# Optimization experiments

Hardware: AMD Instinct MI355X
Metric: run time of the kernel (lower is better)

Reference implementation:

```python
import jax, jax.numpy as jnp
import numpy as np
from jax import lax

B, C, H, W = 8, 384, 32, 32
HEADS, G, STRIDE, KSIZE = 12, 6, 2, 3
HC = C // HEADS          # head channels = 32
CG = C // G              # group channels = 64
NGH = HEADS // G         # heads per group = 2
DEPTHS = 2
D2 = C * 4               # MLP hidden
HK, WK = H // STRIDE, W // STRIDE
NS = HK * WK             # deformable samples = 256
SCALE = HC ** -0.5


def dwconv(x, w, b, stride=1, pad=1):
    # depthwise conv, x:(N,Cx,H,W), w:(Cx,kh,kw)
    c = x.shape[1]
    y = lax.conv_general_dilated(x, w[:, None], (stride, stride),
                                 [(pad, pad), (pad, pad)], feature_group_count=c,
                                 dimension_numbers=('NCHW', 'OIHW', 'NCHW'))
    return y + b[None, :, None, None]


def conv1x1(x, w, b=None):
    y = jnp.einsum('oc,bchw->bohw', w, x)
    return y if b is None else y + b[None, :, None, None]


def layernorm_c(x, w, b, eps=1e-5):
    # LayerNormProxy: LN over channel dim of NCHW
    xt = x.transpose(0, 2, 3, 1)
    mu = xt.mean(-1, keepdims=True)
    var = xt.var(-1, keepdims=True)
    xt = (xt - mu) * lax.rsqrt(var + eps) * w + b
    return xt.transpose(0, 3, 1, 2)


def grid_sample(img, grid):
    # F.grid_sample, bilinear, align_corners=True. img:(N,Ci,Hi,Wi), grid:(N,Hg,Wg,2) as (x,y) in [-1,1]
    N, Ci, Hi, Wi = img.shape
    gx = (grid[..., 0] + 1.0) * 0.5 * (Wi - 1)
    gy = (grid[..., 1] + 1.0) * 0.5 * (Hi - 1)
    x0 = jnp.floor(gx)
    y0 = jnp.floor(gy)
    wx = (gx - x0)[:, None]   # (N,1,Hg,Wg)
    wy = (gy - y0)[:, None]
    x0i = jnp.clip(x0.astype(jnp.int32), 0, Wi - 1)
    y0i = jnp.clip(y0.astype(jnp.int32), 0, Hi - 1)
    x1i = jnp.clip(x0i + 1, 0, Wi - 1)
    y1i = jnp.clip(y0i + 1, 0, Hi - 1)
    gather = jax.vmap(lambda im, yi, xi: im[:, yi, xi])  # -> (N,Ci,Hg,Wg)
    v00 = gather(img, y0i, x0i)
    v01 = gather(img, y0i, x1i)
    v10 = gather(img, y1i, x0i)
    v11 = gather(img, y1i, x1i)
    return (v00 * (1 - wx) * (1 - wy) + v01 * wx * (1 - wy)
            + v10 * (1 - wx) * wy + v11 * wx * wy)


def _norm_grid(hs, ws, centered):
    if centered:  # _get_ref_points
        ys = jnp.linspace(0.5, hs - 0.5, hs)
        xs = jnp.linspace(0.5, ws - 0.5, ws)
    else:         # _get_q_grid
        ys = jnp.arange(hs, dtype=jnp.float32)
        xs = jnp.arange(ws, dtype=jnp.float32)
    ys = ys / (hs - 1.0) * 2.0 - 1.0
    xs = xs / (ws - 1.0) * 2.0 - 1.0
    return jnp.stack(jnp.meshgrid(ys, xs, indexing='ij'), -1)  # (hs,ws,2) (y,x)


def dattn(x, wq, bq, wk, bk, wv, bv, wo, bo, odw, odb, olw, olb, opw, rpe):
    q = conv1x1(x, wq, bq)                              # (B,C,H,W)
    q_off = q.reshape(B * G, CG, H, W)
    off = dwconv(q_off, odw, odb, stride=STRIDE, pad=KSIZE // 2)  # (BG,CG,HK,WK)
    off = jax.nn.gelu(layernorm_c(off, olw, olb), approximate=False)
    off = conv1x1(off, opw).transpose(0, 2, 3, 1)       # (BG,HK,WK,2) as (dy,dx)
    ref = _norm_grid(HK, WK, True)[None]
    pos = jnp.clip(off + ref, -1.0, 1.0)                # (BG,HK,WK,2) (y,x)
    xs = grid_sample(x.reshape(B * G, CG, H, W), pos[..., ::-1])  # (BG,CG,HK,WK)
    xs = xs.reshape(B, C, 1, NS)
    qf = q.reshape(B * HEADS, HC, H * W)
    k = conv1x1(xs, wk, bk).reshape(B * HEADS, HC, NS)
    v = conv1x1(xs, wv, bv).reshape(B * HEADS, HC, NS)
    attn = jnp.einsum('bcm,bcn->bmn', qf, k) * SCALE    # (B*HEADS, HW, NS)
    rpe_g = jnp.broadcast_to(rpe[None], (B,) + rpe.shape).reshape(B * G, NGH, 2 * H - 1, 2 * W - 1)
    qg = _norm_grid(H, W, False).reshape(1, H * W, 2)
    disp = (qg[:, :, None, :] - pos.reshape(B * G, 1, NS, 2)) * 0.5  # (BG,HW,NS,2)
    bias = grid_sample(rpe_g, disp[..., ::-1]).reshape(B * HEADS, H * W, NS)
    attn = jax.nn.softmax(attn + bias, axis=2)
    out = jnp.einsum('bmn,bcn->bcm', attn, v).reshape(B, C, H, W)
    return conv1x1(out, wo, bo)


def _forward(x, lpu_w, lpu_b, wq, bq, wk, bk, wv, bv, wo, bo,
             off_dw_w, off_dw_b, off_ln_w, off_ln_b, off_pw_w, rpe,
             mlp_w1, mlp_b1, mlp_dw_w, mlp_dw_b, mlp_w2, mlp_b2):
    # proj is Identity (dim_in == dim_embed); layer_norms/layer_scales/drop_path are Identity; dropouts are 0
    for d in range(DEPTHS):
        x = x + dwconv(x, lpu_w[d], lpu_b[d])  # local perception unit
        x = x + dattn(x, wq[d], bq[d], wk[d], bk[d], wv[d], bv[d], wo[d], bo[d],
                      off_dw_w[d], off_dw_b[d], off_ln_w[d], off_ln_b[d], off_pw_w[d], rpe[d])
        h = conv1x1(x, mlp_w1[d], mlp_b1[d])
        h = h + dwconv(h, mlp_dw_w[d], mlp_dw_b[d])
        h = jax.nn.gelu(h, approximate=False)
        x = x + conv1x1(h, mlp_w2[d], mlp_b2[d])
    return x


def setup_inputs():
    key = jax.random.key(0)
    ks = iter(jax.random.split(key, 16))
    def p(shape, std=0.02):
        return jax.random.normal(next(ks), shape, jnp.float32) * std
    D = DEPTHS
    return {
        "x": jax.random.normal(next(ks), (B, C, H, W), jnp.float32),
        "lpu_w": p((D, C, 3, 3)), "lpu_b": jnp.zeros((D, C), jnp.float32),
        "wq": p((D, C, C)), "bq": jnp.zeros((D, C), jnp.float32),
        "wk": p((D, C, C)), "bk": jnp.zeros((D, C), jnp.float32),
        "wv": p((D, C, C)), "bv": jnp.zeros((D, C), jnp.float32),
        "wo": p((D, C, C)), "bo": jnp.zeros((D, C), jnp.float32),
        "off_dw_w": p((D, CG, 3, 3)), "off_dw_b": jnp.zeros((D, CG), jnp.float32),
        "off_ln_w": jnp.ones((D, CG), jnp.float32), "off_ln_b": jnp.zeros((D, CG), jnp.float32),
        "off_pw_w": p((D, 2, CG)),
        "rpe": p((D, HEADS, 2 * H - 1, 2 * W - 1), 0.01),
        "mlp_w1": p((D, D2, C)), "mlp_b1": jnp.zeros((D, D2), jnp.float32),
        "mlp_dw_w": p((D, D2, 3, 3)), "mlp_dw_b": jnp.zeros((D, D2), jnp.float32),
        "mlp_w2": p((D, C, D2)), "mlp_b2": jnp.zeros((D, C), jnp.float32),
    }


def reference(x, lpu_w, lpu_b, wq, bq, wk, bk, wv, bv, wo, bo,
              off_dw_w, off_dw_b, off_ln_w, off_ln_b, off_pw_w, rpe,
              mlp_w1, mlp_b1, mlp_dw_w, mlp_dw_b, mlp_w2, mlp_b2):
    return _forward(x, lpu_w, lpu_b, wq, bq, wk, bk, wv, bv, wo, bo,
                    off_dw_w, off_dw_b, off_ln_w, off_ln_b, off_pw_w, rpe,
                    mlp_w1, mlp_b1, mlp_dw_w, mlp_dw_b, mlp_w2, mlp_b2)
```

## Files before the change

### kernel.cpp

```cpp
#include <hip/hip_runtime.h>
#include <hip/hip_bf16.h>
#include <math.h>

namespace {

constexpr int B_ = 8, C_ = 384, H_ = 32, W_ = 32, HW_ = 1024;
constexpr int HEADS_ = 12, G_ = 6, HC_ = 32, CG_ = 64, NS_ = 256, D2_ = 1536;
constexpr float SCALE_ = 0.17677669529663687f;

using short8 = __attribute__((ext_vector_type(8))) short;
using f32x4 = __attribute__((ext_vector_type(4))) float;
using u32x4 = __attribute__((ext_vector_type(4))) unsigned;
typedef unsigned short ushort_t;

__device__ __forceinline__ float gelu_exact(float x) {
  return 0.5f * x * (1.f + erff(x * 0.70710678118654752f));
}
__device__ __forceinline__ ushort_t f2bf(float f) {
  unsigned u = __float_as_uint(f);
  u = (u + 0x7FFFu + ((u >> 16) & 1u)) >> 16;
  return (ushort_t)u;
}
__device__ __forceinline__ float bf2f(ushort_t s) {
  return __uint_as_float(((unsigned)s) << 16);
}
__device__ __forceinline__ float bflo(unsigned u) { return __uint_as_float(u << 16); }
__device__ __forceinline__ float bfhi(unsigned u) { return __uint_as_float(u & 0xFFFF0000u); }
__device__ __forceinline__ unsigned pack2(float a, float b) {
  return (unsigned)f2bf(a) | ((unsigned)f2bf(b) << 16);
}

typedef __attribute__((address_space(1))) const unsigned int gq_u32;
typedef __attribute__((address_space(3))) unsigned int lq_u32;
__device__ __forceinline__ void gload16(const ushort_t* g, ushort_t* l) {
  __builtin_amdgcn_global_load_lds((gq_u32*)g, (lq_u32*)l, 16, 0, 0);
}

__global__ __launch_bounds__(256) void wcvt_rpe(
    const float* __restrict__ s0, const float* __restrict__ s1,
    const float* __restrict__ s2, const float* __restrict__ s3,
    const float* __restrict__ s4, const float* __restrict__ s5,
    ushort_t* __restrict__ dst, const float* __restrict__ rpe,
    uint2* __restrict__ rpq) {
  int blk = blockIdx.x;
  if (blk < 13824) {
    long idx = (long)blk * 256 + threadIdx.x;
    long off = idx;
    const float* s;
    if (off < 294912) s = s0;
    else if ((off -= 294912) < 294912) s = s1;
    else if ((off -= 294912) < 294912) s = s2;
    else if ((off -= 294912) < 294912) s = s3;
    else if ((off -= 294912) < 1179648) s = s4;
    else { off -= 1179648; s = s5; }
    dst[idx] = f2bf(s[off]);
  } else {
    int hb = blk - 13824;
    const float* rph = rpe + (size_t)hb * 3969;
    uint2* dq = rpq + (size_t)hb * 4096;
    for (int i = threadIdx.x; i < 4096; i += 256) {
      int y = i >> 6, x = i & 63;
      float v00 = 0.f, v01 = 0.f, v10 = 0.f, v11 = 0.f;
      if (y < 63) {
        if (x < 63) v00 = rph[y * 63 + x];
        if (x < 62) v01 = rph[y * 63 + x + 1];
      }
      if (y < 62) {
        if (x < 63) v10 = rph[(y + 1) * 63 + x];
        if (x < 62) v11 = rph[(y + 1) * 63 + x + 1];
      }
      dq[i] = make_uint2(pack2(v00, v01), pack2(v10, v11));
    }
  }
}

__global__ __launch_bounds__(256) void dwconv_lpu(
    const float* __restrict__ x, const float* __restrict__ w,
    const float* __restrict__ bias, float* __restrict__ y,
    ushort_t* __restrict__ yt) {
  __shared__ __align__(16) float tile[32][33];
  int hp = blockIdx.x, c0 = blockIdx.y * 32, b = blockIdx.z;
  int t = threadIdx.x;
  int cl = t >> 3, g4 = t & 7;
  int c = c0 + cl;
  const float* img = x + ((size_t)b * C_ + c) * HW_;
  const float* wc = w + c * 9;
  float o0 = bias[c], o1 = o0, o2 = o0, o3 = o0;
#pragma unroll
  for (int ky = 0; ky < 3; ++ky) {
    int ih = hp + ky - 1;
    if ((unsigned)ih >= 32u) continue;
    const float* row = img + ih * 32 + g4 * 4;
    float4 m = *(const float4*)row;
    float v0 = (g4 > 0) ? row[-1] : 0.f;
    float v5 = (g4 < 7) ? row[4] : 0.f;
    float k0 = wc[ky * 3], k1 = wc[ky * 3 + 1], k2 = wc[ky * 3 + 2];
    o0 = fmaf(k0, v0, fmaf(k1, m.x, fmaf(k2, m.y, o0)));
    o1 = fmaf(k0, m.x, fmaf(k1, m.y, fmaf(k2, m.z, o1)));
    o2 = fmaf(k0, m.y, fmaf(k1, m.z, fmaf(k2, m.w, o2)));
    o3 = fmaf(k0, m.z, fmaf(k1, m.w, fmaf(k2, v5, o3)));
  }
  float4 ctr = *(const float4*)(img + hp * 32 + g4 * 4);
  o0 += ctr.x; o1 += ctr.y; o2 += ctr.z; o3 += ctr.w;
  *(float4*)(y + ((size_t)b * C_ + c) * HW_ + hp * 32 + g4 * 4) =
      make_float4(o0, o1, o2, o3);
  tile[cl][g4 * 4 + 0] = o0;
  tile[cl][g4 * 4 + 1] = o1;
  tile[cl][g4 * 4 + 2] = o2;
  tile[cl][g4 * 4 + 3] = o3;
  __syncthreads();
  int wl = t >> 3, cg = t & 7;
  unsigned p0 = pack2(tile[cg * 4 + 0][wl], tile[cg * 4 + 1][wl]);
  unsigned p1 = pack2(tile[cg * 4 + 2][wl], tile[cg * 4 + 3][wl]);
  unsigned* dst = (unsigned*)(yt + ((size_t)b * HW_ + hp * 32 + wl) * C_ + c0 + cg * 4);
  dst[0] = p0;
  dst[1] = p1;
}

__global__ __launch_bounds__(256) void dwgelu_t(
    const ushort_t* __restrict__ hin, const float* __restrict__ w,
    const float* __restrict__ bias, ushort_t* __restrict__ ht) {
  __shared__ __align__(16) float tile[2][32][33];
  int hp0 = blockIdx.x * 2, c0 = blockIdx.y * 32, b = blockIdx.z;
  int t = threadIdx.x;
  int cl = t >> 3, rw = (t >> 2) & 1, g8 = t & 3;
  int hp = hp0 + rw;
  int c = c0 + cl;
  const ushort_t* img = hin + ((size_t)b * D2_ + c) * HW_;
  const float* wc = w + c * 9;
  float o[8];
  float bi = bias[c];
#pragma unroll
  for (int j = 0; j < 8; ++j) o[j] = bi;
#pragma unroll
  for (int ky = 0; ky < 3; ++ky) {
    int ih = hp + ky - 1;
    if ((unsigned)ih >= 32u) continue;
    const ushort_t* row = img + ih * 32 + g8 * 8;
    uint4 u = *(const uint4*)row;
    float vv[10];
    vv[0] = (g8 > 0) ? bf2f(row[-1]) : 0.f;
    vv[1] = bflo(u.x); vv[2] = bfhi(u.x); vv[3] = bflo(u.y); vv[4] = bfhi(u.y);
    vv[5] = bflo(u.z); vv[6] = bfhi(u.z); vv[7] = bflo(u.w); vv[8] = bfhi(u.w);
    vv[9] = (g8 < 3) ? bf2f(row[8]) : 0.f;
    float k0 = wc[ky * 3], k1 = wc[ky * 3 + 1], k2 = wc[ky * 3 + 2];
#pragma unroll
    for (int j = 0; j < 8; ++j)
      o[j] = fmaf(k0, vv[j], fmaf(k1, vv[j + 1], fmaf(k2, vv[j + 2], o[j])));
  }
  {
    uint4 u = *(const uint4*)(img + hp * 32 + g8 * 8);
    float cv[8] = {bflo(u.x), bfhi(u.x), bflo(u.y), bfhi(u.y),
                   bflo(u.z), bfhi(u.z), bflo(u.w), bfhi(u.w)};
#pragma unroll
    for (int j = 0; j < 8; ++j) {
      o[j] += cv[j];
      tile[rw][cl][g8 * 8 + j] = gelu_exact(o[j]);
    }
  }
  __syncthreads();
  int wl = t >> 3, cg = t & 7;
#pragma unroll
  for (int rr = 0; rr < 2; ++rr) {
    unsigned p0 = pack2(tile[rr][cg * 4 + 0][wl], tile[rr][cg * 4 + 1][wl]);
    unsigned p1 = pack2(tile[rr][cg * 4 + 2][wl], tile[rr][cg * 4 + 3][wl]);
    unsigned* dst = (unsigned*)(ht + ((size_t)b * HW_ + (hp0 + rr) * 32 + wl) * D2_ + c0 + cg * 4);
    dst[0] = p0;
    dst[1] = p1;
  }
}

__global__ __launch_bounds__(256) void gemm_kv(
    const ushort_t* __restrict__ Wk, const ushort_t* __restrict__ Wv,
    const ushort_t* __restrict__ Xt, const float* __restrict__ bk,
    const float* __restrict__ bv, ushort_t* __restrict__ ktb,
    ushort_t* __restrict__ vbn) {
  constexpr int K = C_, N = NS_, O = C_;
  struct __align__(16) SMem {
    union {
      struct { char a[8192]; char b[8192]; } st;
      float shuf[64 * 68];
    };
  };
  __shared__ SMem sm;
  int t = threadIdx.x;
  int lane = t & 63, wave = t >> 6;
  int wm = (wave >> 1) * 32, wn = (wave & 1) * 32;
  int bz = blockIdx.z;
  bool isK = blockIdx.y < 6;
  int o0 = (isK ? blockIdx.y : blockIdx.y - 6) * 64;
  int n0 = blockIdx.x * 64;
  const ushort_t* Wb = isK ? Wk : Wv;
  const float* bias = isK ? bk : bv;
  const ushort_t* Ag = Wb + (size_t)o0 * K;
  const ushort_t* Bg = Xt + ((size_t)bz * N + n0) * K;
  int sr = t >> 3, sc = t & 7;
  int swz = ((sc ^ (sr & 7)) << 4);
  f32x4 acc[2][2];
#pragma unroll
  for (int fi = 0; fi < 2; ++fi)
#pragma unroll
    for (int fj = 0; fj < 2; ++fj) acc[fi][fj] = f32x4{0.f, 0.f, 0.f, 0.f};
  int lrow = lane & 15, lk = lane >> 4;
  short8 a0 = *(const short8*)(Ag + (size_t)sr * K + sc * 8);
  short8 a1 = *(const short8*)(Ag + (size_t)(sr + 32) * K + sc * 8);
  short8 b0 = *(const short8*)(Bg + (size_t)sr * K + sc * 8);
  short8 b1 = *(const short8*)(Bg + (size_t)(sr + 32) * K + sc * 8);
  constexpr int NSTEP = K / 64;
#pragma unroll
  for (int s = 0; s < NSTEP; ++s) {
    if (s) __syncthreads();
    *(short8*)(sm.st.a + sr * 128 + swz) = a0;
    *(short8*)(sm.st.a + (sr + 32) * 128 + swz) = a1;
    *(short8*)(sm.st.b + sr * 128 + swz) = b0;
    *(short8*)(sm.st.b + (sr + 32) * 128 + swz) = b1;
    __syncthreads();
    if (s + 1 < NSTEP) {
      int k0 = (s + 1) * 64;
      a0 = *(const short8*)(Ag + (size_t)sr * K + k0 + sc * 8);
      a1 = *(const short8*)(Ag + (size_t)(sr + 32) * K + k0 + sc * 8);
      b0 = *(const short8*)(Bg + (size_t)sr * K + k0 + sc * 8);
      b1 = *(const short8*)(Bg + (size_t)(sr + 32) * K + k0 + sc * 8);
    }
#pragma unroll
    for (int kk = 0; kk < 2; ++kk) {
      short8 af[2], bfr[2];
#pragma unroll
      for (int fi = 0; fi < 2; ++fi) {
        int row = wm + fi * 16 + lrow;
        af[fi] = *(const short8*)(sm.st.a + row * 128 + (((kk * 4 + lk) ^ (row & 7)) << 4));
      }
#pragma unroll
      for (int fj = 0; fj < 2; ++fj) {
        int row = wn + fj * 16 + lrow;
        bfr[fj] = *(const short8*)(sm.st.b + row * 128 + (((kk * 4 + lk) ^ (row & 7)) << 4));
      }
#pragma unroll
      for (int fi = 0; fi < 2; ++fi)
#pragma unroll
        for (int fj = 0; fj < 2; ++fj)
          acc[fi][fj] = __builtin_amdgcn_mfma_f32_16x16x32_bf16(af[fi], bfr[fj], acc[fi][fj], 0, 0, 0);
    }
  }
  __syncthreads();
#pragma unroll
  for (int fi = 0; fi < 2; ++fi) {
#pragma unroll
    for (int r = 0; r < 4; ++r) {
      int ol = wm + fi * 16 + lk * 4 + r;
      float bi = bias[o0 + ol];
#pragma unroll
      for (int fj = 0; fj < 2; ++fj) {
        int nl = wn + fj * 16 + lrow;
        sm.shuf[ol * 68 + nl] = acc[fi][fj][r] + bi;
      }
    }
  }
  __syncthreads();
  if (isK) {
    int nl = t >> 2, og = (t & 3) * 16;
    unsigned pk[8];
#pragma unroll
    for (int i = 0; i < 8; ++i)
      pk[i] = pack2(sm.shuf[(og + 2 * i) * 68 + nl], sm.shuf[(og + 2 * i + 1) * 68 + nl]);
    unsigned* dst = (unsigned*)(ktb + ((size_t)bz * N + (n0 + nl)) * O + o0 + og);
    *(uint4*)(dst) = make_uint4(pk[0], pk[1], pk[2], pk[3]);
    *(uint4*)(dst + 4) = make_uint4(pk[4], pk[5], pk[6], pk[7]);
  } else {
    int ol = t >> 2, ng = (t & 3) * 16;
    unsigned pk[8];
#pragma unroll
    for (int i = 0; i < 8; ++i)
      pk[i] = pack2(sm.shuf[ol * 68 + ng + 2 * i], sm.shuf[ol * 68 + ng + 2 * i + 1]);
    unsigned* dst = (unsigned*)(vbn + ((size_t)bz * O + (o0 + ol)) * N + n0 + ng);
    *(uint4*)(dst) = make_uint4(pk[0], pk[1], pk[2], pk[3]);
    *(uint4*)(dst + 4) = make_uint4(pk[4], pk[5], pk[6], pk[7]);
  }
}

template <int BN, bool F32, bool B16N, bool B16T, bool RES>
__global__ __launch_bounds__(256) void gemm128(
    const ushort_t* __restrict__ Wb, const ushort_t* __restrict__ Xt,
    const float* __restrict__ bias, const float* __restrict__ resid,
    float* __restrict__ Y, ushort_t* __restrict__ Yb, int O, int K, int N) {
  constexpr int MFW = (BN == 128) ? 4 : 2;
  __shared__ __align__(16) ushort_t sA[2][128 * 64];
  __shared__ __align__(16) ushort_t sB[2][BN * 64];
  int t = threadIdx.x;
  int l = t & 63, w = t >> 6;
  int o0 = blockIdx.y * 128, n0 = blockIdx.x * BN, bz = blockIdx.z;
  const ushort_t* Ag = Wb + (size_t)o0 * K;
  const ushort_t* Bg = Xt + ((size_t)bz * N + n0) * K;
  int lr8 = l >> 3;
  int scol = (((l & 7) ^ (lr8 & 7)) * 8);
  int lrow = l & 15, lg = l >> 4;
  int wm = (BN == 128) ? (w >> 1) * 64 : w * 32;
  int wn = (BN == 128) ? (w & 1) * 64 : 0;
  f32x4 acc[MFW][4];
#pragma unroll
  for (int fi = 0; fi < MFW; ++fi)
#pragma unroll
    for (int fj = 0; fj < 4; ++fj) acc[fi][fj] = f32x4{0.f, 0.f, 0.f, 0.f};
  auto stage = [&](int buf, int k0) {
#pragma unroll
    for (int i = 0; i < 4; ++i)
      gload16(Ag + (size_t)(w * 32 + i * 8 + lr8) * K + k0 + scol,
              sA[buf] + (w * 32 + i * 8) * 64);
    if constexpr (BN == 128) {
#pragma unroll
      for (int i = 0; i < 4; ++i)
        gload16(Bg + (size_t)(w * 32 + i * 8 + lr8) * K + k0 + scol,
                sB[buf] + (w * 32 + i * 8) * 64);
    } else {
#pragma unroll
      for (int i = 0; i < 2; ++i)
        gload16(Bg + (size_t)(w * 16 + i * 8 + lr8) * K + k0 + scol,
                sB[buf] + (w * 16 + i * 8) * 64);
    }
  };
  stage(0, 0);
  __syncthreads();
  int nstep = K >> 6;
  for (int s = 0; s < nstep; ++s) {
    int cur = s & 1;
    if (s + 1 < nstep) stage(cur ^ 1, (s + 1) * 64);
#pragma unroll
    for (int kk = 0; kk < 2; ++kk) {
      short8 af[MFW], bfr[4];
#pragma unroll
      for (int fi = 0; fi < MFW; ++fi) {
        int row = wm + fi * 16 + lrow;
        af[fi] = *(const short8*)(sA[cur] + row * 64 + (((kk * 4 + lg) ^ (row & 7)) << 3));
      }
#pragma unroll
      for (int fj = 0; fj < 4; ++fj) {
        int row = wn + fj * 16 + lrow;
        bfr[fj] = *(const short8*)(sB[cur] + row * 64 + (((kk * 4 + lg) ^ (row & 7)) << 3));
      }
#pragma unroll
      for (int fi = 0; fi < MFW; ++fi)
#pragma unroll
        for (int fj = 0; fj < 4; ++fj)
          acc[fi][fj] = __builtin_amdgcn_mfma_f32_16x16x32_bf16(af[fi], bfr[fj], acc[fi][fj], 0, 0, 0);
    }
    __syncthreads();
  }
#pragma unroll
  for (int fi = 0; fi < MFW; ++fi) {
    int ob = wm + fi * 16 + lg * 4;
    float bi[4];
#pragma unroll
    for (int r = 0; r < 4; ++r) bi[r] = bias[o0 + ob + r];
#pragma unroll
    for (int fj = 0; fj < 4; ++fj) {
      int n = n0 + wn + fj * 16 + lrow;
      float v[4];
#pragma unroll
      for (int r = 0; r < 4; ++r) {
        v[r] = acc[fi][fj][r] + bi[r];
        if (RES) v[r] += resid[((size_t)bz * O + ob + r + o0) * N + n];
        if (F32) Y[((size_t)bz * O + ob + r + o0) * N + n] = v[r];
        if (B16N) Yb[((size_t)bz * O + ob + r + o0) * N + n] = f2bf(v[r]);
      }
      if (B16T) {
        uint2 u;
        u.x = pack2(v[0], v[1]);
        u.y = pack2(v[2], v[3]);
        *(uint2*)&Yb[((size_t)bz * N + n) * O + o0 + ob] = u;
      }
    }
  }
}

__global__ __launch_bounds__(256) void offset_kernel(
    const ushort_t* __restrict__ qt, const float* __restrict__ odw,
    const float* __restrict__ odb, const float* __restrict__ olw,
    const float* __restrict__ olb, const float* __restrict__ opw,
    float* __restrict__ pos) {
  int blk = blockIdx.x;
  int bg = blk >> 2, pb = blk & 3;
  int b = bg / G_, g = bg % G_;
  int t = threadIdx.x;
  int p = pb * 64 + (t >> 2);
  int q = t & 3;
  int c0 = q * 16;
  int hk = p >> 4, wk = p & 15;
  const ushort_t* qb = qt + (size_t)b * HW_ * C_ + g * CG_ + c0;
  float sv[16];
#pragma unroll
  for (int j = 0; j < 16; ++j) sv[j] = odb[c0 + j];
#pragma unroll
  for (int ky = 0; ky < 3; ++ky) {
    int ih = 2 * hk + ky - 1;
    if ((unsigned)ih >= 32u) continue;
#pragma unroll
    for (int kx = 0; kx < 3; ++kx) {
      int iw = 2 * wk + kx - 1;
      if ((unsigned)iw >= 32u) continue;
      const ushort_t* qp = qb + (size_t)(ih * 32 + iw) * C_;
      uint4 u0 = *(const uint4*)qp;
      uint4 u1 = *(const uint4*)(qp + 8);
      float vv[16] = {bflo(u0.x), bfhi(u0.x), bflo(u0.y), bfhi(u0.y),
                      bflo(u0.z), bfhi(u0.z), bflo(u0.w), bfhi(u0.w),
                      bflo(u1.x), bfhi(u1.x), bflo(u1.y), bfhi(u1.y),
                      bflo(u1.z), bfhi(u1.z), bflo(u1.w), bfhi(u1.w)};
      int tap = ky * 3 + kx;
#pragma unroll
      for (int j = 0; j < 16; ++j)
        sv[j] = fmaf(odw[(c0 + j) * 9 + tap], vv[j], sv[j]);
    }
  }
  float s1 = 0.f;
#pragma unroll
  for (int j = 0; j < 16; ++j) s1 += sv[j];
  s1 += __shfl_xor(s1, 1);
  s1 += __shfl_xor(s1, 2);
  float mu = s1 * (1.f / CG_);
  float vs = 0.f;
#pragma unroll
  for (int j = 0; j < 16; ++j) {
    float d = sv[j] - mu;
    vs = fmaf(d, d, vs);
  }
  vs += __shfl_xor(vs, 1);
  vs += __shfl_xor(vs, 2);
  float rs = rsqrtf(vs * (1.f / CG_) + 1e-5f);
  float dy = 0.f, dx = 0.f;
#pragma unroll
  for (int j = 0; j < 16; ++j) {
    int c = c0 + j;
    float tv = (sv[j] - mu) * rs * olw[c] + olb[c];
    float ge = gelu_exact(tv);
    dy = fmaf(opw[c], ge, dy);
    dx = fmaf(opw[CG_ + c], ge, dx);
  }
  dy += __shfl_xor(dy, 1);
  dy += __shfl_xor(dy, 2);
  dx += __shfl_xor(dx, 1);
  dx += __shfl_xor(dx, 2);
  if (q == 0) {
    float ry = (hk + 0.5f) * (2.f / 15.f) - 1.f;
    float rx = (wk + 0.5f) * (2.f / 15.f) - 1.f;
    pos[(size_t)bg * 512 + p * 2 + 0] = fminf(fmaxf(dy + ry, -1.f), 1.f);
    pos[(size_t)bg * 512 + p * 2 + 1] = fminf(fmaxf(dx + rx, -1.f), 1.f);
  }
}

__global__ __launch_bounds__(256) void sample_xst(
    const float* __restrict__ y1, const float* __restrict__ pos,
    ushort_t* __restrict__ xst) {
  int bg = blockIdx.y;
  int b = bg / G_, g = bg % G_;
  int t = threadIdx.x;
  int cg = t & 63, nl = t >> 6;
  int n = blockIdx.x * 4 + nl;
  float py = pos[(size_t)bg * 512 + 2 * n];
  float px = pos[(size_t)bg * 512 + 2 * n + 1];
  float gx = (px + 1.f) * 15.5f, gy = (py + 1.f) * 15.5f;
  float fx = floorf(gx), fy = floorf(gy);
  float wx = gx - fx, wy = gy - fy;
  int x0 = min(max((int)fx, 0), 31), y0 = min(max((int)fy, 0), 31);
  int x1 = min(x0 + 1, 31), y1i = min(y0 + 1, 31);
  const float* img = y1 + ((size_t)b * C_ + g * CG_ + cg) * HW_;
  float v00 = img[y0 * 32 + x0], v01 = img[y0 * 32 + x1];
  float v10 = img[y1i * 32 + x0], v11 = img[y1i * 32 + x1];
  float v = v00 * (1.f - wx) * (1.f - wy) + v01 * wx * (1.f - wy) +
            v10 * (1.f - wx) * wy + v11 * wx * wy;
  xst[((size_t)b * NS_ + n) * C_ + g * CG_ + cg] = f2bf(v);
}

__global__ __launch_bounds__(256) void attn_kernel(
    const ushort_t* __restrict__ qt, const ushort_t* __restrict__ kt,
    const ushort_t* __restrict__ vbn, const float* __restrict__ pos,
    const uint2* __restrict__ rpq, ushort_t* __restrict__ aot) {
  __shared__ __align__(16) uint2 sRPQ[4096];
  __shared__ __align__(16) ushort_t sP[4][32 * 40];
  __shared__ unsigned sIB[256];
  __shared__ float sW2[512];
  int bid = blockIdx.x;
  int swzb = (bid & 7) * 96 + (bid >> 3);
  int qb = swzb & 7;
  int grp = swzb >> 3;
  int h = grp % HEADS_;
  int b = grp / HEADS_;
  int t = threadIdx.x;
  int l = t & 63, wv = t >> 6;
  int lrow = l & 15, lg = l >> 4;
  int bg = b * G_ + (h >> 1);
  {
    const ushort_t* src = (const ushort_t*)(rpq + (size_t)h * 4096);
    ushort_t* dstb = (ushort_t*)sRPQ;
#pragma unroll
    for (int i = 0; i < 8; ++i)
      gload16(src + i * 2048 + t * 8, dstb + i * 2048 + wv * 512);
  }
  {
    float py = pos[(size_t)bg * 512 + 2 * t];
    float px = pos[(size_t)bg * 512 + 2 * t + 1];
    float cy = 15.5f - 15.5f * py;
    float cx = 15.5f - 15.5f * px;
    float fy = floorf(cy), fx = floorf(cx);
    sIB[t] = (unsigned)((int)fy * 64 + (int)fx);
    sW2[2 * t] = cy - fy;
    sW2[2 * t + 1] = cx - fx;
  }
  __syncthreads();

  int m0 = qb * 128 + wv * 32;
  short8 qf[2];
  int aq[2];
#pragma unroll
  for (int f = 0; f < 2; ++f) {
    int m = m0 + f * 16 + lrow;
    qf[f] = *(const short8*)(qt + ((size_t)b * HW_ + m) * C_ + h * HC_ + lg * 8);
    aq[f] = (m >> 5) * 64 + (m & 31);
  }
  const ushort_t* kbase = kt + (size_t)b * NS_ * C_ + h * HC_;
  const ushort_t* vbase = vbn + ((size_t)b * C_ + h * HC_) * NS_;
  f32x4 oc[2][2];
#pragma unroll
  for (int f = 0; f < 2; ++f)
#pragma unroll
    for (int ct = 0; ct < 2; ++ct) oc[f][ct] = f32x4{0.f, 0.f, 0.f, 0.f};
  float mrun[2] = {-1e30f, -1e30f}, lrun[2] = {0.f, 0.f};
  ushort_t* sPw = sP[wv];

  for (int c = 0; c < 8; ++c) {
    f32x4 s[2][2];
    __builtin_amdgcn_s_setprio(1);
#pragma unroll
    for (int T = 0; T < 2; ++T) {
      short8 kf = *(const short8*)(kbase + (size_t)((c * 2 + T) * 16 + lrow) * C_ + lg * 8);
#pragma unroll
      for (int f = 0; f < 2; ++f)
        s[f][T] = __builtin_amdgcn_mfma_f32_16x16x32_bf16(kf, qf[f], f32x4{0.f, 0.f, 0.f, 0.f}, 0, 0, 0);
    }
    __builtin_amdgcn_s_setprio(0);
    u32x4 ibT[2];
    f32x4 wA[2], wB[2];
#pragma unroll
    for (int T = 0; T < 2; ++T) {
      int kbase2 = c * 32 + T * 16 + lg * 4;
      ibT[T] = *(const u32x4*)&sIB[kbase2];
      wA[T] = *(const f32x4*)&sW2[2 * kbase2];
      wB[T] = *(const f32x4*)&sW2[2 * kbase2 + 4];
    }
#pragma unroll
    for (int f = 0; f < 2; ++f)
#pragma unroll
      for (int T = 0; T < 2; ++T)
#pragma unroll
        for (int r = 0; r < 4; ++r) {
          int a = aq[f] + (int)ibT[T][r];
          float wy = (r < 2) ? wA[T][(r & 1) * 2] : wB[T][(r & 1) * 2];
          float wx = (r < 2) ? wA[T][(r & 1) * 2 + 1] : wB[T][(r & 1) * 2 + 1];
          uint2 qd = sRPQ[a];
          float b00 = bflo(qd.x), b01 = bfhi(qd.x);
          float b10 = bflo(qd.y), b11 = bfhi(qd.y);
          float r0 = b00 + wx * (b01 - b00);
          float r1 = b10 + wx * (b11 - b10);
          s[f][T][r] = s[f][T][r] * SCALE_ + r0 + wy * (r1 - r0);
        }
#pragma unroll
    for (int f = 0; f < 2; ++f) {
      float mx = s[f][0][0];
#pragma unroll
      for (int T = 0; T < 2; ++T)
#pragma unroll
        for (int r = 0; r < 4; ++r) mx = fmaxf(mx, s[f][T][r]);
      mx = fmaxf(mx, __shfl_xor(mx, 16));
      mx = fmaxf(mx, __shfl_xor(mx, 32));
      if (!__all(mx <= mrun[f] + 8.f)) {
        float newm = fmaxf(mrun[f], mx);
        float fac = __expf(mrun[f] - newm);
        mrun[f] = newm;
        lrun[f] *= fac;
#pragma unroll
        for (int ct = 0; ct < 2; ++ct)
#pragma unroll
          for (int r = 0; r < 4; ++r) oc[f][ct][r] *= fac;
      }
      float ps = 0.f;
#pragma unroll
      for (int T = 0; T < 2; ++T)
#pragma unroll
        for (int r = 0; r < 4; ++r) {
          float p = __expf(s[f][T][r] - mrun[f]);
          s[f][T][r] = p;
          ps += p;
        }
      ps += __shfl_xor(ps, 16);
      ps += __shfl_xor(ps, 32);
      lrun[f] += ps;
#pragma unroll
      for (int T = 0; T < 2; ++T) {
        uint2 u;
        u.x = pack2(s[f][T][0], s[f][T][1]);
        u.y = pack2(s[f][T][2], s[f][T][3]);
        *(uint2*)&sPw[(f * 16 + lrow) * 40 + T * 16 + lg * 4] = u;
      }
    }
    short8 pa[2];
#pragma unroll
    for (int f = 0; f < 2; ++f)
      pa[f] = *(const short8*)&sPw[(f * 16 + lrow) * 40 + lg * 8];
    __builtin_amdgcn_s_setprio(1);
#pragma unroll
    for (int ct = 0; ct < 2; ++ct) {
      short8 vf = *(const short8*)(vbase + (size_t)(ct * 16 + lrow) * NS_ + c * 32 + lg * 8);
#pragma unroll
      for (int f = 0; f < 2; ++f)
        oc[f][ct] = __builtin_amdgcn_mfma_f32_16x16x32_bf16(pa[f], vf, oc[f][ct], 0, 0, 0);
    }
    __builtin_amdgcn_s_setprio(0);
  }
#pragma unroll
  for (int f = 0; f < 2; ++f) {
    float inv = 1.f / lrun[f];
    float invq[4];
#pragma unroll
    for (int r = 0; r < 4; ++r) invq[r] = __shfl(inv, lg * 4 + r);
#pragma unroll
    for (int ct = 0; ct < 2; ++ct)
#pragma unroll
      for (int r = 0; r < 4; ++r) {
        int m = m0 + f * 16 + lg * 4 + r;
        aot[((size_t)b * HW_ + m) * C_ + h * HC_ + ct * 16 + lrow] =
            f2bf(oc[f][ct][r] * invq[r]);
      }
  }
}

}

extern "C" void kernel_launch(void* const* d_in, const int* in_sizes, int n_in,
                              void* d_out, int out_size, void* d_ws,
                              size_t ws_size, hipStream_t stream) {
  const float* x_in = (const float*)d_in[0];
  const float* lpu_w = (const float*)d_in[1];
  const float* lpu_b = (const float*)d_in[2];
  const float* wq = (const float*)d_in[3];
  const float* bq = (const float*)d_in[4];
  const float* wk = (const float*)d_in[5];
  const float* bk = (const float*)d_in[6];
  const float* wv = (const float*)d_in[7];
  const float* bv = (const float*)d_in[8];
  const float* wo = (const float*)d_in[9];
  const float* bo = (const float*)d_in[10];
  const float* odw = (const float*)d_in[11];
  const float* odb = (const float*)d_in[12];
  const float* olw = (const float*)d_in[13];
  const float* olb = (const float*)d_in[14];
  const float* opw = (const float*)d_in[15];
  const float* rpe = (const float*)d_in[16];
  const float* w1 = (const float*)d_in[17];
  const float* b1 = (const float*)d_in[18];
  const float* mdw = (const float*)d_in[19];
  const float* mdb = (const float*)d_in[20];
  const float* w2 = (const float*)d_in[21];
  const float* b2 = (const float*)d_in[22];
  float* out = (float*)d_out;

  constexpr size_t XSZ = (size_t)B_ * C_ * HW_;
  constexpr size_t SSZ = (size_t)B_ * C_ * NS_;
  constexpr size_t HSZ = (size_t)B_ * D2_ * HW_;

  char* base = (char*)d_ws;
  auto alloc = [&](size_t bytes) {
    char* p = base;
    base += (bytes + 255) & ~(size_t)255;
    return p;
  };
  float* bufX = (float*)alloc(XSZ * 4);
  float* y1 = (float*)alloc(XSZ * 4);
  float* x2 = (float*)alloc(XSZ * 4);
  float* pos = (float*)alloc(48 * 512 * 4);
  ushort_t* qt = (ushort_t*)alloc(XSZ * 2);
  ushort_t* tb1 = (ushort_t*)alloc(XSZ * 2);
  ushort_t* aot = (ushort_t*)alloc(XSZ * 2);
  ushort_t* xst = (ushort_t*)alloc(SSZ * 2);
  ushort_t* ktb = (ushort_t*)alloc(SSZ * 2);
  ushort_t* vbn = (ushort_t*)alloc(SSZ * 2);
  ushort_t* h1b = (ushort_t*)alloc(HSZ * 2);
  ushort_t* h3t = (ushort_t*)alloc(HSZ * 2);
  ushort_t* wb = (ushort_t*)alloc((size_t)3538944 * 2);
  uint2* rpq = (uint2*)alloc((size_t)2 * HEADS_ * 4096 * 8);

  ushort_t* wqb = wb;
  ushort_t* wkb = wb + 294912;
  ushort_t* wvb = wb + 589824;
  ushort_t* wob = wb + 884736;
  ushort_t* w1b = wb + 1179648;
  ushort_t* w2b = wb + 2359296;

  wcvt_rpe<<<13824 + 24, 256, 0, stream>>>(wq, wk, wv, wo, w1, w2, wb, rpe, rpq);

  for (int d = 0; d < 2; ++d) {
    const float* xin = (d == 0) ? x_in : bufX;
    float* xnext = (d == 1) ? out : bufX;
    const ushort_t* wqd = wqb + (size_t)d * 147456;
    const ushort_t* wkd = wkb + (size_t)d * 147456;
    const ushort_t* wvd = wvb + (size_t)d * 147456;
    const ushort_t* wod = wob + (size_t)d * 147456;
    const ushort_t* w1d = w1b + (size_t)d * 589824;
    const ushort_t* w2d = w2b + (size_t)d * 589824;

    dwconv_lpu<<<dim3(32, 12, 8), 256, 0, stream>>>(xin, lpu_w + d * C_ * 9,
                                                    lpu_b + d * C_, y1, tb1);
    gemm128<64, false, false, true, false><<<dim3(16, 3, 8), 256, 0, stream>>>(
        wqd, tb1, bq + d * C_, nullptr, nullptr, qt, C_, C_, HW_);
    offset_kernel<<<192, 256, 0, stream>>>(qt, odw + d * CG_ * 9, odb + d * CG_,
                                           olw + d * CG_, olb + d * CG_,
                                           opw + d * 2 * CG_, pos);
    sample_xst<<<dim3(64, 48), 256, 0, stream>>>(y1, pos, xst);
    gemm_kv<<<dim3(4, 12, 8), 256, 0, stream>>>(wkd, wvd, xst, bk + d * C_,
                                                bv + d * C_, ktb, vbn);
    attn_kernel<<<768, 256, 0, stream>>>(qt, ktb, vbn, pos,
                                         rpq + (size_t)d * HEADS_ * 4096, aot);
    gemm128<64, true, false, true, true><<<dim3(16, 3, 8), 256, 0, stream>>>(
        wod, aot, bo + d * C_, y1, x2, tb1, C_, C_, HW_);
    gemm128<128, false, true, false, false><<<dim3(8, 12, 8), 256, 0, stream>>>(
        w1d, tb1, b1 + d * D2_, nullptr, nullptr, h1b, D2_, C_, HW_);
    dwgelu_t<<<dim3(16, 48, 8), 256, 0, stream>>>(h1b, mdw + d * D2_ * 9,
                                                  mdb + d * D2_, h3t);
    gemm128<64, true, false, false, true><<<dim3(16, 3, 8), 256, 0, stream>>>(
        w2d, h3t, b2 + d * C_, x2, xnext, nullptr, C_, D2_, HW_);
  }
}
```

Baseline: 432.6 us.

## Store intermediate residual activations in bf16 and halve RPE table size

Switches the fp32 residual/intermediate activations (y1, x2, block output between depths) to bf16, so the dwconv, sample, output-projection and MLP GEMM epilogues read and write half the bytes. The relative-position table is also stored as single packed pairs, with the second row read from a +64 offset instead of a quad-packed entry, which halves the LDS footprint and the load in the attention kernel. The cost is lower precision on the residual stream and an extra LDS read per bias lookup.

```diff
diff --git a/kernel.cpp b/kernel.cpp
--- a/kernel.cpp
+++ b/kernel.cpp
@@ -41,7 +41,7 @@
     const float* __restrict__ s2, const float* __restrict__ s3,
     const float* __restrict__ s4, const float* __restrict__ s5,
     ushort_t* __restrict__ dst, const float* __restrict__ rpe,
-    uint2* __restrict__ rpq) {
+    unsigned* __restrict__ rp2) {
   int blk = blockIdx.x;
   if (blk < 13824) {
     long idx = (long)blk * 256 + threadIdx.x;
@@ -57,53 +57,64 @@
   } else {
     int hb = blk - 13824;
     const float* rph = rpe + (size_t)hb * 3969;
-    uint2* dq = rpq + (size_t)hb * 4096;
+    unsigned* dq = rp2 + (size_t)hb * 4096;
     for (int i = threadIdx.x; i < 4096; i += 256) {
       int y = i >> 6, x = i & 63;
-      float v00 = 0.f, v01 = 0.f, v10 = 0.f, v11 = 0.f;
+      float v0 = 0.f, v1 = 0.f;
       if (y < 63) {
-        if (x < 63) v00 = rph[y * 63 + x];
-        if (x < 62) v01 = rph[y * 63 + x + 1];
-      }
-      if (y < 62) {
-        if (x < 63) v10 = rph[(y + 1) * 63 + x];
-        if (x < 62) v11 = rph[(y + 1) * 63 + x + 1];
-      }
-      dq[i] = make_uint2(pack2(v00, v01), pack2(v10, v11));
-    }
-  }
-}
-
+        if (x < 63) v0 = rph[y * 63 + x];
+        if (x < 62) v1 = rph[y * 63 + x + 1];
+      }
+      dq[i] = pack2(v0, v1);
+    }
+  }
+}
+
+template <bool INF32>
 __global__ __launch_bounds__(256) void dwconv_lpu(
-    const float* __restrict__ x, const float* __restrict__ w,
-    const float* __restrict__ bias, float* __restrict__ y,
+    const void* __restrict__ xin, const float* __restrict__ w,
+    const float* __restrict__ bias, ushort_t* __restrict__ yb,
     ushort_t* __restrict__ yt) {
   __shared__ __align__(16) float tile[32][33];
   int hp = blockIdx.x, c0 = blockIdx.y * 32, b = blockIdx.z;
   int t = threadIdx.x;
   int cl = t >> 3, g4 = t & 7;
   int c = c0 + cl;
-  const float* img = x + ((size_t)b * C_ + c) * HW_;
   const float* wc = w + c * 9;
   float o0 = bias[c], o1 = o0, o2 = o0, o3 = o0;
+  float m0, m1, m2, m3;
 #pragma unroll
   for (int ky = 0; ky < 3; ++ky) {
     int ih = hp + ky - 1;
     if ((unsigned)ih >= 32u) continue;
-    const float* row = img + ih * 32 + g4 * 4;
-    float4 m = *(const float4*)row;
-    float v0 = (g4 > 0) ? row[-1] : 0.f;
-    float v5 = (g4 < 7) ? row[4] : 0.f;
+    float r0, r1, r2, r3, v0, v5;
+    if (INF32) {
+      const float* img = (const float*)xin + ((size_t)b * C_ + c) * HW_;
+      const float* row = img + ih * 32 + g4 * 4;
+      float4 m = *(const float4*)row;
+      r0 = m.x; r1 = m.y; r2 = m.z; r3 = m.w;
+      v0 = (g4 > 0) ? row[-1] : 0.f;
+      v5 = (g4 < 7) ? row[4] : 0.f;
+    } else {
+      const ushort_t* img = (const ushort_t*)xin + ((size_t)b * C_ + c) * HW_;
+      const ushort_t* row = img + ih * 32 + g4 * 4;
+      uint2 u = *(const uint2*)row;
+      r0 = bflo(u.x); r1 = bfhi(u.x); r2 = bflo(u.y); r3 = bfhi(u.y);
+      v0 = (g4 > 0) ? bf2f(row[-1]) : 0.f;
+      v5 = (g4 < 7) ? bf2f(row[4]) : 0.f;
+    }
     float k0 = wc[ky * 3], k1 = wc[ky * 3 + 1], k2 = wc[ky * 3 + 2];
-    o0 = fmaf(k0, v0, fmaf(k1, m.x, fmaf(k2, m.y, o0)));
-    o1 = fmaf(k0, m.x, fmaf(k1, m.y, fmaf(k2, m.z, o1)));
-    o2 = fmaf(k0, m.y, fmaf(k1, m.z, fmaf(k2, m.w, o2)));
-    o3 = fmaf(k0, m.z, fmaf(k1, m.w, fmaf(k2, v5, o3)));
-  }
-  float4 ctr = *(const float4*)(img + hp * 32 + g4 * 4);
-  o0 += ctr.x; o1 += ctr.y; o2 += ctr.z; o3 += ctr.w;
-  *(float4*)(y + ((size_t)b * C_ + c) * HW_ + hp * 32 + g4 * 4) =
-      make_float4(o0, o1, o2, o3);
+    o0 = fmaf(k0, v0, fmaf(k1, r0, fmaf(k2, r1, o0)));
+    o1 = fmaf(k0, r0, fmaf(k1, r1, fmaf(k2, r2, o1)));
+    o2 = fmaf(k0, r1, fmaf(k1, r2, fmaf(k2, r3, o2)));
+    o3 = fmaf(k0, r2, fmaf(k1, r3, fmaf(k2, v5, o3)));
+    if (ky == 1) { m0 = r0; m1 = r1; m2 = r2; m3 = r3; }
+  }
+  o0 += m0; o1 += m1; o2 += m2; o3 += m3;
+  uint2 pk;
+  pk.x = pack2(o0, o1);
+  pk.y = pack2(o2, o3);
+  *(uint2*)(yb + ((size_t)b * C_ + c) * HW_ + hp * 32 + g4 * 4) = pk;
   tile[cl][g4 * 4 + 0] = o0;
   tile[cl][g4 * 4 + 1] = o1;
   tile[cl][g4 * 4 + 2] = o2;
@@ -281,8 +292,9 @@
 template <int BN, bool F32, bool B16N, bool B16T, bool RES>
 __global__ __launch_bounds__(256) void gemm128(
     const ushort_t* __restrict__ Wb, const ushort_t* __restrict__ Xt,
-    const float* __restrict__ bias, const float* __restrict__ resid,
-    float* __restrict__ Y, ushort_t* __restrict__ Yb, int O, int K, int N) {
+    const float* __restrict__ bias, const ushort_t* __restrict__ residb,
+    float* __restrict__ Y, ushort_t* __restrict__ Yn, ushort_t* __restrict__ Yb,
+    int O, int K, int N) {
   constexpr int MFW = (BN == 128) ? 4 : 2;
   __shared__ __align__(16) ushort_t sA[2][128 * 64];
   __shared__ __align__(16) ushort_t sB[2][BN * 64];
@@ -358,9 +370,9 @@
 #pragma unroll
       for (int r = 0; r < 4; ++r) {
         v[r] = acc[fi][fj][r] + bi[r];
-        if (RES) v[r] += resid[((size_t)bz * O + ob + r + o0) * N + n];
+        if (RES) v[r] += bf2f(residb[((size_t)bz * O + ob + r + o0) * N + n]);
         if (F32) Y[((size_t)bz * O + ob + r + o0) * N + n] = v[r];
-        if (B16N) Yb[((size_t)bz * O + ob + r + o0) * N + n] = f2bf(v[r]);
+        if (B16N) Yn[((size_t)bz * O + ob + r + o0) * N + n] = f2bf(v[r]);
       }
       if (B16T) {
         uint2 u;
@@ -447,7 +459,7 @@
 }
 
 __global__ __launch_bounds__(256) void sample_xst(
-    const float* __restrict__ y1, const float* __restrict__ pos,
+    const ushort_t* __restrict__ y1b, const float* __restrict__ pos,
     ushort_t* __restrict__ xst) {
   int bg = blockIdx.y;
   int b = bg / G_, g = bg % G_;
@@ -461,9 +473,9 @@
   float wx = gx - fx, wy = gy - fy;
   int x0 = min(max((int)fx, 0), 31), y0 = min(max((int)fy, 0), 31);
   int x1 = min(x0 + 1, 31), y1i = min(y0 + 1, 31);
-  const float* img = y1 + ((size_t)b * C_ + g * CG_ + cg) * HW_;
-  float v00 = img[y0 * 32 + x0], v01 = img[y0 * 32 + x1];
-  float v10 = img[y1i * 32 + x0], v11 = img[y1i * 32 + x1];
+  const ushort_t* img = y1b + ((size_t)b * C_ + g * CG_ + cg) * HW_;
+  float v00 = bf2f(img[y0 * 32 + x0]), v01 = bf2f(img[y0 * 32 + x1]);
+  float v10 = bf2f(img[y1i * 32 + x0]), v11 = bf2f(img[y1i * 32 + x1]);
   float v = v00 * (1.f - wx) * (1.f - wy) + v01 * wx * (1.f - wy) +
             v10 * (1.f - wx) * wy + v11 * wx * wy;
   xst[((size_t)b * NS_ + n) * C_ + g * CG_ + cg] = f2bf(v);
@@ -472,8 +484,8 @@
 __global__ __launch_bounds__(256) void attn_kernel(
     const ushort_t* __restrict__ qt, const ushort_t* __restrict__ kt,
     const ushort_t* __restrict__ vbn, const float* __restrict__ pos,
-    const uint2* __restrict__ rpq, ushort_t* __restrict__ aot) {
-  __shared__ __align__(16) uint2 sRPQ[4096];
+    const unsigned* __restrict__ rp2, ushort_t* __restrict__ aot) {
+  __shared__ __align__(16) unsigned sRP2[4096];
   __shared__ __align__(16) ushort_t sP[4][32 * 40];
   __shared__ unsigned sIB[256];
   __shared__ float sW2[512];
@@ -488,10 +500,10 @@
   int lrow = l & 15, lg = l >> 4;
   int bg = b * G_ + (h >> 1);
   {
-    const ushort_t* src = (const ushort_t*)(rpq + (size_t)h * 4096);
-    ushort_t* dstb = (ushort_t*)sRPQ;
-#pragma unroll
-    for (int i = 0; i < 8; ++i)
+    const ushort_t* src = (const ushort_t*)(rp2 + (size_t)h * 4096);
+    ushort_t* dstb = (ushort_t*)sRP2;
+#pragma unroll
+    for (int i = 0; i < 4; ++i)
       gload16(src + i * 2048 + t * 8, dstb + i * 2048 + wv * 512);
   }
   {
@@ -554,9 +566,10 @@
           int a = aq[f] + (int)ibT[T][r];
           float wy = (r < 2) ? wA[T][(r & 1) * 2] : wB[T][(r & 1) * 2];
           float wx = (r < 2) ? wA[T][(r & 1) * 2 + 1] : wB[T][(r & 1) * 2 + 1];
-          uint2 qd = sRPQ[a];
-          float b00 = bflo(qd.x), b01 = bfhi(qd.x);
-          float b10 = bflo(qd.y), b11 = bfhi(qd.y);
+          unsigned top = sRP2[a];
+          unsigned bot = sRP2[a + 64];
+          float b00 = bflo(top), b01 = bfhi(top);
+          float b10 = bflo(bot), b11 = bfhi(bot);
           float r0 = b00 + wx * (b01 - b00);
           float r1 = b10 + wx * (b11 - b10);
           s[f][T][r] = s[f][T][r] * SCALE_ + r0 + wy * (r1 - r0);
@@ -671,9 +684,9 @@
     base += (bytes + 255) & ~(size_t)255;
     return p;
   };
-  float* bufX = (float*)alloc(XSZ * 4);
-  float* y1 = (float*)alloc(XSZ * 4);
-  float* x2 = (float*)alloc(XSZ * 4);
+  ushort_t* bufXb = (ushort_t*)alloc(XSZ * 2);
+  ushort_t* y1b = (ushort_t*)alloc(XSZ * 2);
+  ushort_t* x2b = (ushort_t*)alloc(XSZ * 2);
   float* pos = (float*)alloc(48 * 512 * 4);
   ushort_t* qt = (ushort_t*)alloc(XSZ * 2);
   ushort_t* tb1 = (ushort_t*)alloc(XSZ * 2);
@@ -684,7 +697,7 @@
   ushort_t* h1b = (ushort_t*)alloc(HSZ * 2);
   ushort_t* h3t = (ushort_t*)alloc(HSZ * 2);
   ushort_t* wb = (ushort_t*)alloc((size_t)3538944 * 2);
-  uint2* rpq = (uint2*)alloc((size_t)2 * HEADS_ * 4096 * 8);
+  unsigned* rp2 = (unsigned*)alloc((size_t)2 * HEADS_ * 4096 * 4);
 
   ushort_t* wqb = wb;
   ushort_t* wkb = wb + 294912;
@@ -693,11 +706,9 @@
   ushort_t* w1b = wb + 1179648;
   ushort_t* w2b = wb + 2359296;
 
-  wcvt_rpe<<<13824 + 24, 256, 0, stream>>>(wq, wk, wv, wo, w1, w2, wb, rpe, rpq);
+  wcvt_rpe<<<13824 + 24, 256, 0, stream>>>(wq, wk, wv, wo, w1, w2, wb, rpe, rp2);
 
   for (int d = 0; d < 2; ++d) {
-    const float* xin = (d == 0) ? x_in : bufX;
-    float* xnext = (d == 1) ? out : bufX;
     const ushort_t* wqd = wqb + (size_t)d * 147456;
     const ushort_t* wkd = wkb + (size_t)d * 147456;
     const ushort_t* wvd = wvb + (size_t)d * 147456;
@@ -705,25 +716,33 @@
     const ushort_t* w1d = w1b + (size_t)d * 589824;
     const ushort_t* w2d = w2b + (size_t)d * 589824;
 
-    dwconv_lpu<<<dim3(32, 12, 8), 256, 0, stream>>>(xin, lpu_w + d * C_ * 9,
-                                                    lpu_b + d * C_, y1, tb1);
+    if (d == 0)
+      dwconv_lpu<true><<<dim3(32, 12, 8), 256, 0, stream>>>(
+          x_in, lpu_w + d * C_ * 9, lpu_b + d * C_, y1b, tb1);
+    else
+      dwconv_lpu<false><<<dim3(32, 12, 8), 256, 0, stream>>>(
+          bufXb, lpu_w + d * C_ * 9, lpu_b + d * C_, y1b, tb1);
     gemm128<64, false, false, true, false><<<dim3(16, 3, 8), 256, 0, stream>>>(
-        wqd, tb1, bq + d * C_, nullptr, nullptr, qt, C_, C_, HW_);
+        wqd, tb1, bq + d * C_, nullptr, nullptr, nullptr, qt, C_, C_, HW_);
     offset_kernel<<<192, 256, 0, stream>>>(qt, odw + d * CG_ * 9, odb + d * CG_,
                                            olw + d * CG_, olb + d * CG_,
                                            opw + d * 2 * CG_, pos);
-    sample_xst<<<dim3(64, 48), 256, 0, stream>>>(y1, pos, xst);
+    sample_xst<<<dim3(64, 48), 256, 0, stream>>>(y1b, pos, xst);
     gemm_kv<<<dim3(4, 12, 8), 256, 0, stream>>>(wkd, wvd, xst, bk + d * C_,
                                                 bv + d * C_, ktb, vbn);
     attn_kernel<<<768, 256, 0, stream>>>(qt, ktb, vbn, pos,
-                                         rpq + (size_t)d * HEADS_ * 4096, aot);
-    gemm128<64, true, false, true, true><<<dim3(16, 3, 8), 256, 0, stream>>>(
-        wod, aot, bo + d * C_, y1, x2, tb1, C_, C_, HW_);
+                                         rp2 + (size_t)d * HEADS_ * 4096, aot);
+    gemm128<64, false, true, true, true><<<dim3(16, 3, 8), 256, 0, stream>>>(
+        wod, aot, bo + d * C_, y1b, nullptr, x2b, tb1, C_, C_, HW_);
     gemm128<128, false, true, false, false><<<dim3(8, 12, 8), 256, 0, stream>>>(
-        w1d, tb1, b1 + d * D2_, nullptr, nullptr, h1b, D2_, C_, HW_);
+        w1d, tb1, b1 + d * D2_, nullptr, nullptr, h1b, nullptr, D2_, C_, HW_);
     dwgelu_t<<<dim3(16, 48, 8), 256, 0, stream>>>(h1b, mdw + d * D2_ * 9,
                                                   mdb + d * D2_, h3t);
-    gemm128<64, true, false, false, true><<<dim3(16, 3, 8), 256, 0, stream>>>(
-        w2d, h3t, b2 + d * C_, x2, xnext, nullptr, C_, D2_, HW_);
-  }
-}
+    if (d == 0)
+      gemm128<64, false, true, false, true><<<dim3(16, 3, 8), 256, 0, stream>>>(
+          w2d, h3t, b2 + d * C_, x2b, nullptr, bufXb, nullptr, C_, D2_, HW_);
+    else
+      gemm128<64, true, false, false, true><<<dim3(16, 3, 8), 256, 0, stream>>>(
+          w2d, h3t, b2 + d * C_, x2b, out, nullptr, nullptr, C_, D2_, HW_);
+  }
+}
```

After: 415.5 us. 4.0% less time.
